# Performance work log

Hardware: AMD Instinct MI355X
Metric: run time of the kernel (lower is better)

Reference implementation:

```python
import jax, jax.numpy as jnp
import numpy as np

B, N, D, U = 8, 2048, 512, 128


def setup_inputs() -> dict:
    key = jax.random.key(0)
    k_x, k_q, k_k, k_v, k_o = jax.random.split(key, 5)
    scale_in = 1.0 / np.sqrt(D)
    scale_u = 1.0 / np.sqrt(U)
    return {
        "inputs": jax.random.normal(k_x, (B, N, D), dtype=jnp.float32),
        "W_q": jax.random.normal(k_q, (D, U), dtype=jnp.float32) * scale_in,
        "W_k": jax.random.normal(k_k, (D, U), dtype=jnp.float32) * scale_in,
        "W_v": jax.random.normal(k_v, (D, U), dtype=jnp.float32) * scale_in,
        "W_o": jax.random.normal(k_o, (U, D), dtype=jnp.float32) * scale_u,
        "b_o": jnp.zeros((D,), dtype=jnp.float32),
    }


def reference(inputs, W_q, W_k, W_v, W_o, b_o):
    # Single-head scaled dot-product self-attention + output dense + residual
    Q = jnp.einsum('bnd,du->bnu', inputs, W_q)
    K = jnp.einsum('bnd,du->bnu', inputs, W_k)
    V = jnp.einsum('bnd,du->bnu', inputs, W_v)
    inv_sqrt_u = 1.0 / jnp.sqrt(jnp.asarray(W_q.shape[-1], inputs.dtype))
    scores = jnp.einsum('bnu,bmu->bnm', Q, K) * inv_sqrt_u  # [B,N,N]
    attn = jax.nn.softmax(scores, axis=-1)
    ctx = jnp.einsum('bnm,bmu->bnu', attn, V)  # [B,N,U]
    return jnp.einsum('bnu,ud->bnd', ctx, W_o) + b_o + inputs
```

## Files before the change

kernel.cpp:

```cpp
#include <hip/hip_runtime.h>

#define BB 8
#define NN 2048
#define DD 512
#define UU 128
#define SPLITS 8
#define KSPLIT 256

typedef __bf16 bf16_t;
typedef __bf16 bf16x4 __attribute__((ext_vector_type(4)));
typedef __bf16 bf16x8 __attribute__((ext_vector_type(8)));
typedef float floatx4 __attribute__((ext_vector_type(4)));

__device__ __forceinline__ floatx4 mfma16(bf16x8 a, bf16x8 b, floatx4 c) {
  return __builtin_amdgcn_mfma_f32_16x16x32_bf16(a, b, c, 0, 0, 0);
}

#define SW(r, g) ((((g) ^ ((r) & 7)) * 8))

__device__ __forceinline__ void gld_lds16(const bf16_t* g, bf16_t* l) {
  __builtin_amdgcn_global_load_lds(
      (const __attribute__((address_space(1))) unsigned int*)g,
      (__attribute__((address_space(3))) unsigned int*)l, 16, 0, 0);
}

__global__ __launch_bounds__(256) void cast_x_kernel(const float* __restrict__ x,
                                                     bf16_t* __restrict__ xb) {
  int G = blockIdx.x * 256 + threadIdx.x;
  int token = G >> 6;
  int g = G & 63;
  int dstg = (g & 56) | ((g & 7) ^ (token & 7));
  const float4* src = reinterpret_cast<const float4*>(x) + (size_t)G * 2;
  float4 a = src[0], b = src[1];
  bf16x8 o;
  o[0] = (bf16_t)a.x; o[1] = (bf16_t)a.y; o[2] = (bf16_t)a.z; o[3] = (bf16_t)a.w;
  o[4] = (bf16_t)b.x; o[5] = (bf16_t)b.y; o[6] = (bf16_t)b.z; o[7] = (bf16_t)b.w;
  *reinterpret_cast<bf16x8*>(&xb[(size_t)token * 512 + dstg * 8]) = o;
}

__global__ __launch_bounds__(256) void pack_w_kernel(const float* __restrict__ wq,
                                                     const float* __restrict__ wk,
                                                     const float* __restrict__ wv,
                                                     const float* __restrict__ wo,
                                                     bf16_t* __restrict__ wqkvt,
                                                     bf16_t* __restrict__ wot) {
  int gid = blockIdx.x * 256 + threadIdx.x;
  if (gid < 384 * 512) {
    int nrow = gid >> 9;
    int kdst = gid & 511;
    int ksrc = (kdst & ~56) | (((((kdst >> 3) & 7)) ^ (nrow & 7)) << 3);
    const float* src = (nrow < 128) ? wq : ((nrow < 256) ? wk : wv);
    int n = nrow & 127;
    wqkvt[gid] = (bf16_t)src[ksrc * 128 + n];
  } else {
    int g = gid - 384 * 512;
    int nrow = g >> 7;
    int kdst = g & 127;
    int ksrc = (kdst & ~56) | (((((kdst >> 3) & 7)) ^ (nrow & 7)) << 3);
    wot[g] = (bf16_t)wo[ksrc * 512 + nrow];
  }
}

__global__ __launch_bounds__(256, 4) void qkv_gemm_kernel(const bf16_t* __restrict__ xb,
                                                          const bf16_t* __restrict__ wqkvt,
                                                          bf16_t* __restrict__ Q,
                                                          bf16_t* __restrict__ K,
                                                          bf16_t* __restrict__ Vt) {
  __shared__ bf16_t lA[64 * 64];
  __shared__ bf16_t lB[64 * 64];
  const int m0 = blockIdx.x * 64;
  const int n0 = blockIdx.y * 64;
  const int tid = threadIdx.x;
  const int w = tid >> 6, lane = tid & 63;
  const int quad = lane >> 4, l15 = lane & 15;

  floatx4 zero4 = {0.f, 0.f, 0.f, 0.f};
  floatx4 acc[4];
#pragma unroll
  for (int nt = 0; nt < 4; nt++) acc[nt] = zero4;

  for (int kc = 0; kc < 512; kc += 64) {
    __syncthreads();
#pragma unroll
    for (int i = 0; i < 2; i++) {
      int t = tid + i * 256;
      int r = t >> 3, g = t & 7;
      gld_lds16(&xb[(size_t)(m0 + r) * 512 + kc + g * 8], &lA[t * 8]);
      gld_lds16(&wqkvt[(size_t)(n0 + r) * 512 + kc + g * 8], &lB[t * 8]);
    }
    asm volatile("s_waitcnt vmcnt(0)" ::: "memory");
    __syncthreads();
#pragma unroll
    for (int kb = 0; kb < 2; kb++) {
      bf16x8 a = *reinterpret_cast<const bf16x8*>(&lA[(w * 16 + l15) * 64 + SW(l15, kb * 4 + quad)]);
#pragma unroll
      for (int nt = 0; nt < 4; nt++) {
        bf16x8 b = *reinterpret_cast<const bf16x8*>(&lB[(nt * 16 + l15) * 64 + SW(l15, kb * 4 + quad)]);
        acc[nt] = mfma16(a, b, acc[nt]);
      }
    }
  }

#pragma unroll
  for (int nt = 0; nt < 4; nt++) {
    int n = n0 + nt * 16 + l15;
#pragma unroll
    for (int r = 0; r < 4; r++) {
      int token = m0 + w * 16 + quad * 4 + r;
      bf16_t h = (bf16_t)acc[nt][r];
      if (n < 128) {
        Q[(size_t)token * 128 + n] = h;
      } else if (n < 256) {
        int nk = n - 128;
        int nsw = (nk & ~56) | ((((nk >> 3) & 7) ^ (token & 7)) << 3);
        K[(size_t)token * 128 + nsw] = h;
      } else {
        int b = token >> 11;
        int t = token & 2047;
        int u = n - 256;
        int tsw = (t & ~56) | ((((t >> 3) & 7) ^ (u & 7)) << 3);
        Vt[((size_t)b * 128 + u) * 2048 + tsw] = h;
      }
    }
  }
}

__global__ __launch_bounds__(256, 3) void attn_kernel(const bf16_t* __restrict__ Q,
                                                      const bf16_t* __restrict__ K,
                                                      const bf16_t* __restrict__ Vt,
                                                      bf16_t* __restrict__ Op,
                                                      float* __restrict__ ml) {
  __shared__ bf16_t lK[64 * 128];
  __shared__ bf16_t lV[128 * 64];
  __shared__ bf16_t lP[4][32 * 64];

  const int b = blockIdx.y;
  const int qb = blockIdx.x;
  const int s = blockIdx.z;
  const int tid = threadIdx.x;
  const int w = tid >> 6, lane = tid & 63;
  const int quad = lane >> 4, l15 = lane & 15;
  const float c = 0.08838834764831845f * 1.4426950408889634f;

  bf16x8 qf[2][4];
#pragma unroll
  for (int mt = 0; mt < 2; mt++) {
    const bf16_t* qrow =
        &Q[((size_t)b * NN + qb * 128 + w * 32 + mt * 16 + l15) * 128 + quad * 8];
#pragma unroll
    for (int kb = 0; kb < 4; kb++)
      qf[mt][kb] = *reinterpret_cast<const bf16x8*>(qrow + kb * 32);
  }

  float l_part[2] = {0.f, 0.f};
  floatx4 zero4 = {0.f, 0.f, 0.f, 0.f};
  floatx4 accO[2][8];
#pragma unroll
  for (int mt = 0; mt < 2; mt++)
#pragma unroll
    for (int ut = 0; ut < 8; ut++) accO[mt][ut] = zero4;

  bf16_t* pw = &lP[w][0];
  const int kt0 = s * KSPLIT;
  for (int kt = kt0; kt < kt0 + KSPLIT; kt += 64) {
    __syncthreads();
    {
      const bf16_t* ksrc = &K[((size_t)b * NN + kt) * 128];
#pragma unroll
      for (int i = 0; i < 4; i++) {
        int t = tid + i * 256;
        gld_lds16(ksrc + (size_t)t * 8, &lK[t * 8]);
      }
      const bf16_t* vbase = &Vt[(size_t)b * 128 * 2048 + kt];
#pragma unroll
      for (int i = 0; i < 4; i++) {
        int t = tid + i * 256;
        int r = t >> 3, g = t & 7;
        gld_lds16(vbase + (size_t)r * 2048 + g * 8, &lV[t * 8]);
      }
    }
    asm volatile("s_waitcnt vmcnt(0)" ::: "memory");
    __syncthreads();

    floatx4 accS[4][2];
#pragma unroll
    for (int km = 0; km < 4; km++)
#pragma unroll
      for (int mt = 0; mt < 2; mt++) accS[km][mt] = zero4;
#pragma unroll
    for (int kb = 0; kb < 4; kb++) {
#pragma unroll
      for (int km = 0; km < 4; km++) {
        bf16x8 kf = *reinterpret_cast<const bf16x8*>(
            &lK[(km * 16 + l15) * 128 + SW(l15, kb * 4 + quad)]);
#pragma unroll
        for (int mt = 0; mt < 2; mt++)
          accS[km][mt] = mfma16(kf, qf[mt][kb], accS[km][mt]);
      }
    }

#pragma unroll
    for (int km = 0; km < 4; km++) {
#pragma unroll
      for (int mt = 0; mt < 2; mt++) {
        float p0 = __builtin_amdgcn_exp2f(accS[km][mt][0] * c);
        float p1 = __builtin_amdgcn_exp2f(accS[km][mt][1] * c);
        float p2 = __builtin_amdgcn_exp2f(accS[km][mt][2] * c);
        float p3 = __builtin_amdgcn_exp2f(accS[km][mt][3] * c);
        l_part[mt] += (p0 + p1) + (p2 + p3);
        bf16x4 pk;
        pk[0] = (bf16_t)p0; pk[1] = (bf16_t)p1; pk[2] = (bf16_t)p2; pk[3] = (bf16_t)p3;
        int row = mt * 16 + l15;
        int g = km * 2 + (quad >> 1);
        *reinterpret_cast<bf16x4*>(
            &pw[row * 64 + ((g ^ (row & 7)) * 8) + (quad & 1) * 4]) = pk;
      }
    }
    asm volatile("s_waitcnt lgkmcnt(0)" ::: "memory");

#pragma unroll
    for (int kb = 0; kb < 2; kb++) {
      bf16x8 pa[2];
#pragma unroll
      for (int mt = 0; mt < 2; mt++)
        pa[mt] = *reinterpret_cast<const bf16x8*>(
            &pw[(mt * 16 + l15) * 64 + SW(l15, kb * 4 + quad)]);
#pragma unroll
      for (int ut = 0; ut < 8; ut++) {
        bf16x8 bv = *reinterpret_cast<const bf16x8*>(
            &lV[(ut * 16 + l15) * 64 + SW(l15, kb * 4 + quad)]);
#pragma unroll
        for (int mt = 0; mt < 2; mt++)
          accO[mt][ut] = mfma16(pa[mt], bv, accO[mt][ut]);
      }
    }
  }

#pragma unroll
  for (int mt = 0; mt < 2; mt++) {
    float v = l_part[mt];
    v += __shfl_xor(v, 16);
    v += __shfl_xor(v, 32);
    l_part[mt] = v;
  }

  size_t base = ((size_t)(b * 16 + qb) * SPLITS + s);
  bf16_t* op = Op + base * (128 * 128);
  float* mlp = ml + base * 128;
#pragma unroll
  for (int mt = 0; mt < 2; mt++)
#pragma unroll
    for (int ut = 0; ut < 8; ut++)
#pragma unroll
      for (int r = 0; r < 4; r++)
        op[(w * 32 + mt * 16 + quad * 4 + r) * 128 + ut * 16 + l15] =
            (bf16_t)accO[mt][ut][r];
  if (quad == 0) {
#pragma unroll
    for (int mt = 0; mt < 2; mt++) mlp[w * 32 + mt * 16 + l15] = l_part[mt];
  }
}

__global__ __launch_bounds__(256) void merge_kernel(const bf16_t* __restrict__ Op,
                                                    const float* __restrict__ ml,
                                                    bf16_t* __restrict__ ctx) {
  const int blk = blockIdx.x;
  const int q = threadIdx.x >> 1;
  const int u0 = blockIdx.y * 64 + (threadIdx.x & 1) * 32;

  float L = 0.f;
  float o[32];
#pragma unroll
  for (int j = 0; j < 32; j++) o[j] = 0.f;
#pragma unroll
  for (int s = 0; s < SPLITS; s++) {
    L += ml[((size_t)blk * SPLITS + s) * 128 + q];
    const bf16_t* op = Op + ((size_t)blk * SPLITS + s) * 16384 + q * 128 + u0;
#pragma unroll
    for (int v = 0; v < 4; v++) {
      bf16x8 ch = *reinterpret_cast<const bf16x8*>(op + v * 8);
#pragma unroll
      for (int j = 0; j < 8; j++) o[v * 8 + j] += (float)ch[j];
    }
  }
  float inv = 1.0f / L;
  const int bb = blk >> 4, qbl = blk & 15;
  bf16_t* dst = ctx + ((size_t)bb * NN + qbl * 128 + q) * 128;
#pragma unroll
  for (int v = 0; v < 4; v++) {
    int g = (u0 >> 3) + v;
    int gsw = (g & 8) | ((g & 7) ^ (q & 7));
    bf16x8 ch;
#pragma unroll
    for (int j = 0; j < 8; j++) ch[j] = (bf16_t)(o[v * 8 + j] * inv);
    *reinterpret_cast<bf16x8*>(dst + gsw * 8) = ch;
  }
}

__global__ __launch_bounds__(256, 4) void out_gemm_kernel(const bf16_t* __restrict__ ctx,
                                                          const bf16_t* __restrict__ wot,
                                                          const float* __restrict__ bo,
                                                          const float* __restrict__ x0,
                                                          float* __restrict__ out) {
  __shared__ bf16_t lA[64 * 128];
  __shared__ bf16_t lB[64 * 128];
  const int m0 = blockIdx.x * 64;
  const int n0 = blockIdx.y * 64;
  const int tid = threadIdx.x;
  const int w = tid >> 6, lane = tid & 63;
  const int quad = lane >> 4, l15 = lane & 15;

#pragma unroll
  for (int i = 0; i < 4; i++) {
    int t = tid + i * 256;
    gld_lds16(&ctx[(size_t)m0 * 128 + t * 8], &lA[t * 8]);
    gld_lds16(&wot[(size_t)n0 * 128 + t * 8], &lB[t * 8]);
  }
  asm volatile("s_waitcnt vmcnt(0)" ::: "memory");
  __syncthreads();

  floatx4 zero4 = {0.f, 0.f, 0.f, 0.f};
  floatx4 acc[4];
#pragma unroll
  for (int nt = 0; nt < 4; nt++) acc[nt] = zero4;
#pragma unroll
  for (int kb = 0; kb < 4; kb++) {
    bf16x8 a = *reinterpret_cast<const bf16x8*>(&lA[(w * 16 + l15) * 128 + SW(l15, kb * 4 + quad)]);
#pragma unroll
    for (int nt = 0; nt < 4; nt++) {
      bf16x8 bfr = *reinterpret_cast<const bf16x8*>(&lB[(nt * 16 + l15) * 128 + SW(l15, kb * 4 + quad)]);
      acc[nt] = mfma16(a, bfr, acc[nt]);
    }
  }

#pragma unroll
  for (int nt = 0; nt < 4; nt++) {
    int n = n0 + nt * 16 + l15;
    float bias = bo[n];
#pragma unroll
    for (int r = 0; r < 4; r++) {
      size_t m = m0 + w * 16 + quad * 4 + r;
      out[m * 512 + n] = acc[nt][r] + bias + x0[m * 512 + n];
    }
  }
}

extern "C" void kernel_launch(void* const* d_in, const int* in_sizes, int n_in,
                              void* d_out, int out_size, void* d_ws, size_t ws_size,
                              hipStream_t stream) {
  const float* x  = (const float*)d_in[0];
  const float* wq = (const float*)d_in[1];
  const float* wk = (const float*)d_in[2];
  const float* wv = (const float*)d_in[3];
  const float* wo = (const float*)d_in[4];
  const float* bo = (const float*)d_in[5];
  float* out = (float*)d_out;

  char* ws = (char*)d_ws;
  bf16_t* Qb    = (bf16_t*)(ws);
  bf16_t* Kb    = (bf16_t*)(ws + 4194304);
  bf16_t* Vt    = (bf16_t*)(ws + 2 * 4194304);
  bf16_t* Ctx   = (bf16_t*)(ws + 3 * 4194304);
  bf16_t* Wqkvt = (bf16_t*)(ws + 4 * 4194304);
  bf16_t* Wot   = (bf16_t*)(ws + 4 * 4194304 + 393216);
  bf16_t* Xb    = (bf16_t*)(ws + 4 * 4194304 + 524288);
  bf16_t* Op    = (bf16_t*)(ws + 4 * 4194304 + 524288);
  float*  ml    = (float*)(ws + 4 * 4194304 + 524288 + 33554432);

  cast_x_kernel<<<4096, 256, 0, stream>>>(x, Xb);
  pack_w_kernel<<<1024, 256, 0, stream>>>(wq, wk, wv, wo, Wqkvt, Wot);
  qkv_gemm_kernel<<<dim3(256, 6), 256, 0, stream>>>(Xb, Wqkvt, Qb, Kb, Vt);
  attn_kernel<<<dim3(16, 8, SPLITS), 256, 0, stream>>>(Qb, Kb, Vt, Op, ml);
  merge_kernel<<<dim3(128, 2), 256, 0, stream>>>(Op, ml, Ctx);
  out_gemm_kernel<<<dim3(256, 8), 256, 0, stream>>>(Ctx, Wot, bo, x, out);
}
```

Baseline: 165.2 us.

## Double-buffer K/V tiles in attention, halve KV splits, enlarge QKV GEMM tile

The attention kernel now prefetches the next K/V tile into a second LDS buffer while computing on the current one, and raises wave priority around MFMA sections. The number of KV splits is halved so each block processes twice as many keys, reducing partial-output traffic and merge work. The QKV projection GEMM computes 128-row tiles per block, reusing B fragments across two M subtiles. The cost is doubled LDS use per attention block, lower occupancy, and fewer blocks in flight.

```diff
diff --git a/kernel.cpp b/kernel.cpp
--- a/kernel.cpp
+++ b/kernel.cpp
@@ -4,8 +4,8 @@
 #define NN 2048
 #define DD 512
 #define UU 128
-#define SPLITS 8
-#define KSPLIT 256
+#define SPLITS 4
+#define KSPLIT 512
 
 typedef __bf16 bf16_t;
 typedef __bf16 bf16x4 __attribute__((ext_vector_type(4)));
@@ -66,72 +66,88 @@
                                                           bf16_t* __restrict__ Q,
                                                           bf16_t* __restrict__ K,
                                                           bf16_t* __restrict__ Vt) {
-  __shared__ bf16_t lA[64 * 64];
+  __shared__ bf16_t lA[128 * 64];
   __shared__ bf16_t lB[64 * 64];
-  const int m0 = blockIdx.x * 64;
+  const int m0 = blockIdx.x * 128;
   const int n0 = blockIdx.y * 64;
   const int tid = threadIdx.x;
   const int w = tid >> 6, lane = tid & 63;
   const int quad = lane >> 4, l15 = lane & 15;
 
   floatx4 zero4 = {0.f, 0.f, 0.f, 0.f};
-  floatx4 acc[4];
-#pragma unroll
-  for (int nt = 0; nt < 4; nt++) acc[nt] = zero4;
+  floatx4 acc[2][4];
+#pragma unroll
+  for (int mi = 0; mi < 2; mi++)
+#pragma unroll
+    for (int nt = 0; nt < 4; nt++) acc[mi][nt] = zero4;
 
   for (int kc = 0; kc < 512; kc += 64) {
     __syncthreads();
+#pragma unroll
+    for (int i = 0; i < 4; i++) {
+      int t = tid + i * 256;
+      int r = t >> 3, g = t & 7;
+      gld_lds16(&xb[(size_t)(m0 + r) * 512 + kc + g * 8], &lA[t * 8]);
+    }
 #pragma unroll
     for (int i = 0; i < 2; i++) {
       int t = tid + i * 256;
       int r = t >> 3, g = t & 7;
-      gld_lds16(&xb[(size_t)(m0 + r) * 512 + kc + g * 8], &lA[t * 8]);
       gld_lds16(&wqkvt[(size_t)(n0 + r) * 512 + kc + g * 8], &lB[t * 8]);
     }
     asm volatile("s_waitcnt vmcnt(0)" ::: "memory");
     __syncthreads();
 #pragma unroll
     for (int kb = 0; kb < 2; kb++) {
-      bf16x8 a = *reinterpret_cast<const bf16x8*>(&lA[(w * 16 + l15) * 64 + SW(l15, kb * 4 + quad)]);
-#pragma unroll
-      for (int nt = 0; nt < 4; nt++) {
-        bf16x8 b = *reinterpret_cast<const bf16x8*>(&lB[(nt * 16 + l15) * 64 + SW(l15, kb * 4 + quad)]);
-        acc[nt] = mfma16(a, b, acc[nt]);
-      }
-    }
-  }
-
-#pragma unroll
-  for (int nt = 0; nt < 4; nt++) {
-    int n = n0 + nt * 16 + l15;
-#pragma unroll
-    for (int r = 0; r < 4; r++) {
-      int token = m0 + w * 16 + quad * 4 + r;
-      bf16_t h = (bf16_t)acc[nt][r];
-      if (n < 128) {
-        Q[(size_t)token * 128 + n] = h;
-      } else if (n < 256) {
-        int nk = n - 128;
-        int nsw = (nk & ~56) | ((((nk >> 3) & 7) ^ (token & 7)) << 3);
-        K[(size_t)token * 128 + nsw] = h;
-      } else {
-        int b = token >> 11;
-        int t = token & 2047;
-        int u = n - 256;
-        int tsw = (t & ~56) | ((((t >> 3) & 7) ^ (u & 7)) << 3);
-        Vt[((size_t)b * 128 + u) * 2048 + tsw] = h;
-      }
-    }
-  }
-}
-
-__global__ __launch_bounds__(256, 3) void attn_kernel(const bf16_t* __restrict__ Q,
+      bf16x8 bfr[4];
+#pragma unroll
+      for (int nt = 0; nt < 4; nt++)
+        bfr[nt] = *reinterpret_cast<const bf16x8*>(
+            &lB[(nt * 16 + l15) * 64 + SW(l15, kb * 4 + quad)]);
+#pragma unroll
+      for (int mi = 0; mi < 2; mi++) {
+        bf16x8 a = *reinterpret_cast<const bf16x8*>(
+            &lA[(w * 32 + mi * 16 + l15) * 64 + SW(l15, kb * 4 + quad)]);
+#pragma unroll
+        for (int nt = 0; nt < 4; nt++)
+          acc[mi][nt] = mfma16(a, bfr[nt], acc[mi][nt]);
+      }
+    }
+  }
+
+#pragma unroll
+  for (int mi = 0; mi < 2; mi++)
+#pragma unroll
+    for (int nt = 0; nt < 4; nt++) {
+      int n = n0 + nt * 16 + l15;
+#pragma unroll
+      for (int r = 0; r < 4; r++) {
+        int token = m0 + w * 32 + mi * 16 + quad * 4 + r;
+        bf16_t h = (bf16_t)acc[mi][nt][r];
+        if (n < 128) {
+          Q[(size_t)token * 128 + n] = h;
+        } else if (n < 256) {
+          int nk = n - 128;
+          int nsw = (nk & ~56) | ((((nk >> 3) & 7) ^ (token & 7)) << 3);
+          K[(size_t)token * 128 + nsw] = h;
+        } else {
+          int bidx = token >> 11;
+          int t = token & 2047;
+          int u = n - 256;
+          int tsw = (t & ~56) | ((((t >> 3) & 7) ^ (u & 7)) << 3);
+          Vt[((size_t)bidx * 128 + u) * 2048 + tsw] = h;
+        }
+      }
+    }
+}
+
+__global__ __launch_bounds__(256, 2) void attn_kernel(const bf16_t* __restrict__ Q,
                                                       const bf16_t* __restrict__ K,
                                                       const bf16_t* __restrict__ Vt,
                                                       bf16_t* __restrict__ Op,
                                                       float* __restrict__ ml) {
-  __shared__ bf16_t lK[64 * 128];
-  __shared__ bf16_t lV[128 * 64];
+  __shared__ bf16_t lK[2][64 * 128];
+  __shared__ bf16_t lV[2][128 * 64];
   __shared__ bf16_t lP[4][32 * 64];
 
   const int b = blockIdx.y;
@@ -162,42 +178,62 @@
 
   bf16_t* pw = &lP[w][0];
   const int kt0 = s * KSPLIT;
+  const bf16_t* kbase = &K[(size_t)b * NN * 128];
+  const bf16_t* vbase = &Vt[(size_t)b * 128 * 2048];
+
+  {
+    const bf16_t* ksrc = kbase + (size_t)kt0 * 128;
+#pragma unroll
+    for (int i = 0; i < 4; i++) {
+      int t = tid + i * 256;
+      gld_lds16(ksrc + (size_t)t * 8, &lK[0][t * 8]);
+    }
+#pragma unroll
+    for (int i = 0; i < 4; i++) {
+      int t = tid + i * 256;
+      int r = t >> 3, g = t & 7;
+      gld_lds16(vbase + (size_t)r * 2048 + kt0 + g * 8, &lV[0][t * 8]);
+    }
+  }
+  asm volatile("s_waitcnt vmcnt(0)" ::: "memory");
+  __syncthreads();
+
+  int cur = 0;
   for (int kt = kt0; kt < kt0 + KSPLIT; kt += 64) {
-    __syncthreads();
-    {
-      const bf16_t* ksrc = &K[((size_t)b * NN + kt) * 128];
+    if (kt + 64 < kt0 + KSPLIT) {
+      const int nxt = kt + 64;
+      const bf16_t* ksrc = kbase + (size_t)nxt * 128;
 #pragma unroll
       for (int i = 0; i < 4; i++) {
         int t = tid + i * 256;
-        gld_lds16(ksrc + (size_t)t * 8, &lK[t * 8]);
-      }
-      const bf16_t* vbase = &Vt[(size_t)b * 128 * 2048 + kt];
+        gld_lds16(ksrc + (size_t)t * 8, &lK[cur ^ 1][t * 8]);
+      }
 #pragma unroll
       for (int i = 0; i < 4; i++) {
         int t = tid + i * 256;
         int r = t >> 3, g = t & 7;
-        gld_lds16(vbase + (size_t)r * 2048 + g * 8, &lV[t * 8]);
-      }
-    }
-    asm volatile("s_waitcnt vmcnt(0)" ::: "memory");
-    __syncthreads();
+        gld_lds16(vbase + (size_t)r * 2048 + nxt + g * 8, &lV[cur ^ 1][t * 8]);
+      }
+    }
 
     floatx4 accS[4][2];
 #pragma unroll
     for (int km = 0; km < 4; km++)
 #pragma unroll
       for (int mt = 0; mt < 2; mt++) accS[km][mt] = zero4;
+    __builtin_amdgcn_s_setprio(1);
 #pragma unroll
     for (int kb = 0; kb < 4; kb++) {
 #pragma unroll
       for (int km = 0; km < 4; km++) {
         bf16x8 kf = *reinterpret_cast<const bf16x8*>(
-            &lK[(km * 16 + l15) * 128 + SW(l15, kb * 4 + quad)]);
+            &lK[cur][(km * 16 + l15) * 128 + SW(l15, kb * 4 + quad)]);
 #pragma unroll
         for (int mt = 0; mt < 2; mt++)
           accS[km][mt] = mfma16(kf, qf[mt][kb], accS[km][mt]);
       }
     }
+    __builtin_amdgcn_s_setprio(0);
 
 #pragma unroll
     for (int km = 0; km < 4; km++) {
@@ -218,6 +254,7 @@
     }
     asm volatile("s_waitcnt lgkmcnt(0)" ::: "memory");
 
+    __builtin_amdgcn_s_setprio(1);
 #pragma unroll
     for (int kb = 0; kb < 2; kb++) {
       bf16x8 pa[2];
@@ -228,12 +265,17 @@
 #pragma unroll
       for (int ut = 0; ut < 8; ut++) {
         bf16x8 bv = *reinterpret_cast<const bf16x8*>(
-            &lV[(ut * 16 + l15) * 64 + SW(l15, kb * 4 + quad)]);
+            &lV[cur][(ut * 16 + l15) * 64 + SW(l15, kb * 4 + quad)]);
 #pragma unroll
         for (int mt = 0; mt < 2; mt++)
           accO[mt][ut] = mfma16(pa[mt], bv, accO[mt][ut]);
       }
     }
+    __builtin_amdgcn_s_setprio(0);
+
+    asm volatile("s_waitcnt vmcnt(0)" ::: "memory");
+    __syncthreads();
+    cur ^= 1;
   }
 
 #pragma unroll
@@ -369,7 +411,7 @@
 
   cast_x_kernel<<<4096, 256, 0, stream>>>(x, Xb);
   pack_w_kernel<<<1024, 256, 0, stream>>>(wq, wk, wv, wo, Wqkvt, Wot);
-  qkv_gemm_kernel<<<dim3(256, 6), 256, 0, stream>>>(Xb, Wqkvt, Qb, Kb, Vt);
+  qkv_gemm_kernel<<<dim3(128, 6), 256, 0, stream>>>(Xb, Wqkvt, Qb, Kb, Vt);
   attn_kernel<<<dim3(16, 8, SPLITS), 256, 0, stream>>>(Qb, Kb, Vt, Op, ml);
   merge_kernel<<<dim3(128, 2), 256, 0, stream>>>(Op, ml, Ctx);
   out_gemm_kernel<<<dim3(256, 8), 256, 0, stream>>>(Ctx, Wot, bo, x, out);
```

Result: faster. 147.6 us (-10.6%).
